# Kernel optimization log

Hardware: AMD Instinct MI355X
Metric: run time of the kernel (lower is better)

## Reference

```python
import jax, jax.numpy as jnp
import numpy as np

H, DH = 4, 64          # heads, dim_head (match init_kwargs)
E = 128                # edge_dim
INNER = H * DH
NEG = -jnp.finfo(jnp.float32).max


def setup_inputs() -> dict:
    key = jax.random.key(0)
    ks = jax.random.split(key, 8)
    b, i, j = 1, 256, 256
    s = lambda fan_in: 1.0 / np.sqrt(fan_in)
    return {
        "inter_edges": jax.random.normal(ks[0], (b, i, j, E), jnp.float32),
        "ab_mask": jnp.ones((b, i), dtype=bool),
        "at_mask": jnp.ones((b, j), dtype=bool),
        "Wq": jax.random.normal(ks[1], (E, INNER), jnp.float32) * s(E),
        "Wk": jax.random.normal(ks[2], (E, INNER), jnp.float32) * s(E),
        "Wv": jax.random.normal(ks[3], (E, INNER), jnp.float32) * s(E),
        "Web": jax.random.normal(ks[4], (E, H), jnp.float32) * s(E),
        "Wg": jax.random.normal(ks[5], (E, INNER), jnp.float32) * s(E),
        "bg": jnp.zeros((INNER,), jnp.float32),
        "Wo": jax.random.normal(ks[6], (INNER, E), jnp.float32) * s(INNER),
        "bo": jnp.zeros((E,), jnp.float32),
    }


def reference(inter_edges, ab_mask, at_mask, Wq, Wk, Wv, Web, Wg, bg, Wo, bo):
    b, i, j, e = inter_edges.shape  # b must be 1 (bias broadcast in original)

    def split_hd(t):  # 'b i j (h d) -> (b h) i j d'
        return t.reshape(b, i, j, H, DH).transpose(0, 3, 1, 2, 4).reshape(b * H, i, j, DH)

    q = split_hd(inter_edges @ Wq)
    k = split_hd(inter_edges @ Wk)
    v = split_hd(inter_edges @ Wv)

    # to_ebias: [b,i,j,h].transpose(0,-1) -> [h,i,j,b]; broadcasts over key axis (b==1)
    z_bias = jnp.swapaxes(inter_edges @ Web, 0, -1)

    # gate uses (d h) split order, unlike q/k/v's (h d)
    gate = jax.nn.sigmoid(inter_edges @ Wg + bg)
    z_gate = gate.reshape(b, i, j, DH, H).transpose(0, 4, 1, 2, 3).reshape(b * H, i, j, DH)

    sim = jnp.einsum('hijd,hikd->hijk', q, k) * (DH ** -0.5) + z_bias

    mask = ab_mask[:, :, None] & at_mask[:, None, :]          # [b,i,j]
    mask = jnp.repeat(mask, H, axis=0)                        # [(b h),i,j]
    sim = jnp.where(mask[..., None], sim, NEG)                # mask whole (i,j) query rows

    attn = jax.nn.softmax(sim, axis=-1)
    # original einsum 'h i j k, h i j d -> h i j d' == v * attn.sum(-1)
    out = v * jnp.sum(attn, axis=-1, keepdims=True)
    out = z_gate * out
    out = out.reshape(b, H, i, j, DH).transpose(0, 2, 3, 1, 4).reshape(b, i, j, INNER)
    return out @ Wo + bo
```

## Files before the change

### kernel.cpp

```cpp
#include <hip/hip_runtime.h>
#include <hip/hip_bf16.h>

typedef __attribute__((ext_vector_type(8))) short short8;
typedef __attribute__((ext_vector_type(4))) float f32x4;

__device__ __forceinline__ unsigned short f2b(float x) {
  union { float f; unsigned u; } v; v.f = x;
  unsigned r = v.u + 0x7fffu + ((v.u >> 16) & 1u);
  return (unsigned short)(r >> 16);
}

__device__ __forceinline__ ushort4 pack4(float4 f) {
  union { __hip_bfloat162 h[2]; ushort4 s; } u;
  u.h[0] = __float22bfloat162_rn(float2{f.x, f.y});
  u.h[1] = __float22bfloat162_rn(float2{f.z, f.w});
  return u.s;
}

__global__ __launch_bounds__(256) void prep_kernel(
    const float* __restrict__ Wv, const float* __restrict__ Wg,
    const float* __restrict__ bgv, const float* __restrict__ Wo,
    unsigned short* __restrict__ W1T, unsigned short* __restrict__ WoT,
    float* __restrict__ bg2)
{
  int t = blockIdx.x * 256 + threadIdx.x;
  if (t < 32768) {
    int e = t >> 8, c = t & 255;
    W1T[c * 128 + e] = f2b(Wv[t]);
  } else if (t < 65536) {
    int s = t - 32768;
    int e = s >> 8, g = s & 255;
    int cc = ((g & 3) << 6) + (g >> 2);
    W1T[(256 + cc) * 128 + e] = f2b(Wg[s]);
  } else if (t < 65536 + 32768) {
    int s = t - 65536;
    int c = s >> 7, o = s & 127;
    WoT[o * 256 + c] = f2b(Wo[s]);
  } else if (t < 65536 + 32768 + 256) {
    int g = t - (65536 + 32768);
    bg2[((g & 3) << 6) + (g >> 2)] = bgv[g];
  }
}

__global__ __launch_bounds__(512, 2) void fused_kernel(
    const float* __restrict__ X,
    const unsigned short* __restrict__ W1T,
    const unsigned short* __restrict__ WoT,
    const float* __restrict__ bg2,
    const float* __restrict__ bo,
    float* __restrict__ Out)
{
  __shared__ unsigned short Xs[2][32 * 128];
  __shared__ unsigned short Ys[2][32 * 256];

  const int tid  = threadIdx.x;
  const int lane = tid & 63;
  const int wave = tid >> 6;
  const int l15  = lane & 15;
  const int lhi  = lane >> 4;
  const long rowbase0 = (long)blockIdx.x * 256;

  short8 wS1[2][4][2];
  float  bgt[2];
  #pragma unroll
  for (int t = 0; t < 2; ++t) {
    int c0 = (wave * 2 + t) * 16;
    const unsigned short* base = W1T + (c0 + l15) * 128 + lhi * 8;
    #pragma unroll
    for (int ks = 0; ks < 4; ++ks) {
      wS1[t][ks][0] = *reinterpret_cast<const short8*>(base + ks * 32);
      wS1[t][ks][1] = *reinterpret_cast<const short8*>(base + ks * 32 + 256 * 128);
    }
    bgt[t] = bg2[c0 + l15];
  }
  short8 wS2[8];
  const int o0 = wave * 16;
  #pragma unroll
  for (int ks = 0; ks < 8; ++ks)
    wS2[ks] = *reinterpret_cast<const short8*>(WoT + (o0 + l15) * 256 + ks * 32 + lhi * 8);
  const float bov = bo[o0 + l15];

  {
    const float4* Xp = reinterpret_cast<const float4*>(X + rowbase0 * 128);
    #pragma unroll
    for (int it = 0; it < 2; ++it) {
      int idx4 = it * 512 + tid;
      float4 f = Xp[idx4];
      int row = idx4 >> 5;
      int col = (idx4 & 31) * 4;
      int sidx = (row * 128 + col) ^ ((row & 7) << 3);
      *reinterpret_cast<ushort4*>(&Xs[0][sidx]) = pack4(f);
    }
  }
  __syncthreads();

  const f32x4 vzero = {0.f, 0.f, 0.f, 0.f};

  for (int i = 0; i < 8; ++i) {
    const int cur = i & 1;

    short8 afrag[2][4];
    #pragma unroll
    for (int mt = 0; mt < 2; ++mt) {
      int row = mt * 16 + l15;
      #pragma unroll
      for (int ks = 0; ks < 4; ++ks) {
        int sidx = (row * 128 + ks * 32 + lhi * 8) ^ ((row & 7) << 3);
        afrag[mt][ks] = *reinterpret_cast<const short8*>(&Xs[cur][sidx]);
      }
    }

    float4 f0, f1;
    if (i < 7) {
      const float4* Xp = reinterpret_cast<const float4*>(X + (rowbase0 + (i + 1) * 32) * 128);
      f0 = Xp[tid];
      f1 = Xp[512 + tid];
    }

    #pragma unroll
    for (int t = 0; t < 2; ++t) {
      int c0 = (wave * 2 + t) * 16;
      f32x4 accV[2] = {vzero, vzero}, accG[2] = {vzero, vzero};
      #pragma unroll
      for (int ks = 0; ks < 4; ++ks) {
        #pragma unroll
        for (int mt = 0; mt < 2; ++mt) {
          accV[mt] = __builtin_amdgcn_mfma_f32_16x16x32_bf16(afrag[mt][ks], wS1[t][ks][0], accV[mt], 0, 0, 0);
          accG[mt] = __builtin_amdgcn_mfma_f32_16x16x32_bf16(afrag[mt][ks], wS1[t][ks][1], accG[mt], 0, 0, 0);
        }
      }
      #pragma unroll
      for (int mt = 0; mt < 2; ++mt) {
        #pragma unroll
        for (int r = 0; r < 4; ++r) {
          int row = mt * 16 + lhi * 4 + r;
          float z = accG[mt][r] + bgt[t];
          float g = 1.0f / (1.0f + __expf(-z));
          float y = g * accV[mt][r];
          int sidx = (row * 256 + c0 + l15) ^ ((row & 7) << 3);
          Ys[cur][sidx] = f2b(y);
        }
      }
    }

    if (i < 7) {
      int idx4 = tid;
      int row = idx4 >> 5, col = (idx4 & 31) * 4;
      int sidx = (row * 128 + col) ^ ((row & 7) << 3);
      *reinterpret_cast<ushort4*>(&Xs[cur ^ 1][sidx]) = pack4(f0);
      idx4 = 512 + tid;
      row = idx4 >> 5; col = (idx4 & 31) * 4;
      sidx = (row * 128 + col) ^ ((row & 7) << 3);
      *reinterpret_cast<ushort4*>(&Xs[cur ^ 1][sidx]) = pack4(f1);
    }

    __syncthreads();

    f32x4 acc2[2] = {vzero, vzero};
    #pragma unroll
    for (int ks = 0; ks < 8; ++ks) {
      #pragma unroll
      for (int mt = 0; mt < 2; ++mt) {
        int row = mt * 16 + l15;
        int sidx = (row * 256 + ks * 32 + lhi * 8) ^ ((row & 7) << 3);
        short8 a = *reinterpret_cast<const short8*>(&Ys[cur][sidx]);
        acc2[mt] = __builtin_amdgcn_mfma_f32_16x16x32_bf16(a, wS2[ks], acc2[mt], 0, 0, 0);
      }
    }
    const long rowb = rowbase0 + (long)i * 32;
    #pragma unroll
    for (int mt = 0; mt < 2; ++mt) {
      #pragma unroll
      for (int r = 0; r < 4; ++r) {
        Out[(rowb + mt * 16 + lhi * 4 + r) * 128 + o0 + l15] = acc2[mt][r] + bov;
      }
    }
  }
}

extern "C" void kernel_launch(void* const* d_in, const int* in_sizes, int n_in,
                              void* d_out, int out_size, void* d_ws, size_t ws_size,
                              hipStream_t stream) {
  const float* X   = (const float*)d_in[0];
  const float* Wv  = (const float*)d_in[5];
  const float* Wg  = (const float*)d_in[7];
  const float* bg  = (const float*)d_in[8];
  const float* Wo  = (const float*)d_in[9];
  const float* bo  = (const float*)d_in[10];

  unsigned short* W1T = (unsigned short*)d_ws;
  unsigned short* WoT = W1T + 512 * 128;
  float*          bg2 = (float*)(WoT + 128 * 256);

  prep_kernel<<<386, 256, 0, stream>>>(Wv, Wg, bg, Wo, W1T, WoT, bg2);

  float* Out = (float*)d_out;
  fused_kernel<<<256, 512, 0, stream>>>(X, W1T, WoT, bg2, bo, Out);
}
```

Baseline: 122.4 us.

## Prefetch input tiles two iterations ahead and raise wave priority during MFMA

Deepens the global-load pipeline for X to two tiles ahead, held in a register double-buffer, so each load has a full iteration of compute to hide its latency. The main loop is now fully unrolled so the buffer indices become compile-time constants. The first GEMM's accumulators for both column tiles are computed before the sigmoid epilogue, and that MFMA block is wrapped in s_setprio. The changes cost extra VGPRs for the buffered float4s and accumulators, which could spill or cut occupancy under the (512,2) launch bounds.

```diff
diff --git a/kernel.cpp b/kernel.cpp
--- a/kernel.cpp
+++ b/kernel.cpp
@@ -80,24 +80,33 @@
     wS2[ks] = *reinterpret_cast<const short8*>(WoT + (o0 + l15) * 256 + ks * 32 + lhi * 8);
   const float bov = bo[o0 + l15];
 
+  const int r0 = tid >> 5,        c0v = (tid & 31) * 4;
+  const int s0w = (r0 * 128 + c0v) ^ ((r0 & 7) << 3);
+  const int r1 = (512 + tid) >> 5, c1v = (tid & 31) * 4;
+  const int s1w = (r1 * 128 + c1v) ^ ((r1 & 7) << 3);
+
   {
     const float4* Xp = reinterpret_cast<const float4*>(X + rowbase0 * 128);
-    #pragma unroll
-    for (int it = 0; it < 2; ++it) {
-      int idx4 = it * 512 + tid;
-      float4 f = Xp[idx4];
-      int row = idx4 >> 5;
-      int col = (idx4 & 31) * 4;
-      int sidx = (row * 128 + col) ^ ((row & 7) << 3);
-      *reinterpret_cast<ushort4*>(&Xs[0][sidx]) = pack4(f);
-    }
+    float4 a = Xp[tid], b = Xp[512 + tid];
+    *reinterpret_cast<ushort4*>(&Xs[0][s0w]) = pack4(a);
+    *reinterpret_cast<ushort4*>(&Xs[0][s1w]) = pack4(b);
+  }
+  float4 pf[2][2];
+  {
+    const float4* Xp = reinterpret_cast<const float4*>(X + (rowbase0 + 32) * 128);
+    pf[1][0] = Xp[tid]; pf[1][1] = Xp[512 + tid];
+  }
+  {
+    const float4* Xp = reinterpret_cast<const float4*>(X + (rowbase0 + 64) * 128);
+    pf[0][0] = Xp[tid]; pf[0][1] = Xp[512 + tid];
   }
   __syncthreads();
 
   const f32x4 vzero = {0.f, 0.f, 0.f, 0.f};
 
+  #pragma unroll
   for (int i = 0; i < 8; ++i) {
-    const int cur = i & 1;
+    const int cb = i & 1;
 
     short8 afrag[2][4];
     #pragma unroll
@@ -106,52 +115,52 @@
       #pragma unroll
       for (int ks = 0; ks < 4; ++ks) {
         int sidx = (row * 128 + ks * 32 + lhi * 8) ^ ((row & 7) << 3);
-        afrag[mt][ks] = *reinterpret_cast<const short8*>(&Xs[cur][sidx]);
-      }
-    }
-
-    float4 f0, f1;
-    if (i < 7) {
-      const float4* Xp = reinterpret_cast<const float4*>(X + (rowbase0 + (i + 1) * 32) * 128);
-      f0 = Xp[tid];
-      f1 = Xp[512 + tid];
-    }
-
+        afrag[mt][ks] = *reinterpret_cast<const short8*>(&Xs[cb][sidx]);
+      }
+    }
+
+    __builtin_amdgcn_s_setprio(1);
+    f32x4 accV[2][2], accG[2][2];
     #pragma unroll
     for (int t = 0; t < 2; ++t) {
-      int c0 = (wave * 2 + t) * 16;
-      f32x4 accV[2] = {vzero, vzero}, accG[2] = {vzero, vzero};
+      #pragma unroll
+      for (int mt = 0; mt < 2; ++mt) { accV[t][mt] = vzero; accG[t][mt] = vzero; }
       #pragma unroll
       for (int ks = 0; ks < 4; ++ks) {
         #pragma unroll
         for (int mt = 0; mt < 2; ++mt) {
-          accV[mt] = __builtin_amdgcn_mfma_f32_16x16x32_bf16(afrag[mt][ks], wS1[t][ks][0], accV[mt], 0, 0, 0);
-          accG[mt] = __builtin_amdgcn_mfma_f32_16x16x32_bf16(afrag[mt][ks], wS1[t][ks][1], accG[mt], 0, 0, 0);
+          accV[t][mt] = __builtin_amdgcn_mfma_f32_16x16x32_bf16(afrag[mt][ks], wS1[t][ks][0], accV[t][mt], 0, 0, 0);
+          accG[t][mt] = __builtin_amdgcn_mfma_f32_16x16x32_bf16(afrag[mt][ks], wS1[t][ks][1], accG[t][mt], 0, 0, 0);
         }
       }
+    }
+    __builtin_amdgcn_s_setprio(0);
+    #pragma unroll
+    for (int t = 0; t < 2; ++t) {
+      int c0 = (wave * 2 + t) * 16;
       #pragma unroll
       for (int mt = 0; mt < 2; ++mt) {
         #pragma unroll
         for (int r = 0; r < 4; ++r) {
           int row = mt * 16 + lhi * 4 + r;
-          float z = accG[mt][r] + bgt[t];
+          float z = accG[t][mt][r] + bgt[t];
           float g = 1.0f / (1.0f + __expf(-z));
-          float y = g * accV[mt][r];
+          float y = g * accV[t][mt][r];
           int sidx = (row * 256 + c0 + l15) ^ ((row & 7) << 3);
-          Ys[cur][sidx] = f2b(y);
+          Ys[cb][sidx] = f2b(y);
         }
       }
     }
 
     if (i < 7) {
-      int idx4 = tid;
-      int row = idx4 >> 5, col = (idx4 & 31) * 4;
-      int sidx = (row * 128 + col) ^ ((row & 7) << 3);
-      *reinterpret_cast<ushort4*>(&Xs[cur ^ 1][sidx]) = pack4(f0);
-      idx4 = 512 + tid;
-      row = idx4 >> 5; col = (idx4 & 31) * 4;
-      sidx = (row * 128 + col) ^ ((row & 7) << 3);
-      *reinterpret_cast<ushort4*>(&Xs[cur ^ 1][sidx]) = pack4(f1);
+      const int ps = (i + 1) & 1;
+      float4 a = pf[ps][0], b = pf[ps][1];
+      *reinterpret_cast<ushort4*>(&Xs[ps][s0w]) = pack4(a);
+      *reinterpret_cast<ushort4*>(&Xs[ps][s1w]) = pack4(b);
+      if (i < 5) {
+        const float4* Xp = reinterpret_cast<const float4*>(X + (rowbase0 + (long)(i + 3) * 32) * 128);
+        pf[ps][0] = Xp[tid]; pf[ps][1] = Xp[512 + tid];
+      }
     }
 
     __syncthreads();
@@ -163,7 +172,7 @@
       for (int mt = 0; mt < 2; ++mt) {
         int row = mt * 16 + l15;
         int sidx = (row * 256 + ks * 32 + lhi * 8) ^ ((row & 7) << 3);
-        short8 a = *reinterpret_cast<const short8*>(&Ys[cur][sidx]);
+        short8 a = *reinterpret_cast<const short8*>(&Ys[cb][sidx]);
         acc2[mt] = __builtin_amdgcn_mfma_f32_16x16x32_bf16(a, wS2[ks], acc2[mt], 0, 0, 0);
       }
     }
```

New measurement: 135.0 us. 1.1x slower.
